# Kernel tuning notes

Hardware: AMD Instinct MI355X
Metric: run time of the kernel (lower is better)

## Reference

```python
import jax, jax.numpy as jnp
import numpy as np

N_NODES = 50000
NODE_IN, NODE_OUT, EDGE_IN = 128, 64, 32
N_EDGES = 400000
ALPHA = 0.2  # LeakyReLU negative slope
EPS = 1e-12  # F.normalize clamp


def setup_inputs() -> dict:
    key = jax.random.key(0)
    ks = jax.random.split(key, 6)
    node_fts = jax.random.normal(ks[0], (N_NODES, NODE_IN), dtype=jnp.float32)
    edge_fts = jax.random.normal(ks[1], (N_EDGES, EDGE_IN), dtype=jnp.float32)
    edges = jax.random.randint(ks[2], (2, N_EDGES), 0, N_NODES)
    # W_node: Linear(node_in, node_out); store weight as [in, out] for x @ W
    W = jax.random.normal(ks[3], (NODE_IN, NODE_OUT), dtype=jnp.float32) * (1.414 * (6.0 / (NODE_IN + NODE_OUT)) ** 0.5)
    b = jnp.zeros((NODE_OUT,), dtype=jnp.float32)
    a_node = jax.random.normal(ks[4], (2 * NODE_OUT + EDGE_IN, 1), dtype=jnp.float32) * 0.1
    scale = jnp.ones((), dtype=jnp.float32)  # MessageNorm learned scale
    return {"node_fts": node_fts, "edge_fts": edge_fts, "edges": edges,
            "W": W, "b": b, "a_node": a_node, "scale": scale}


def reference(node_fts, edge_fts, edges, W, b, a_node, scale):
    # edges: [2, E] -> reshape (row-major, as in torch) to [E, 2]
    e = edges.reshape(-1, 2)                                  # [E, 2]
    eu = jnp.concatenate([e, e[:, ::-1]], axis=0)             # undirected [2E, 2]
    ef_u = jnp.concatenate([edge_fts, edge_fts], axis=0)      # [2E, edge_in]
    src, dst = eu[:, 0], eu[:, 1]

    h_v = node_fts @ W + b                                    # [N, out]

    # per-edge attention logits: cat(h_src, h_dst, edge_ft) @ a
    feat = jnp.concatenate([h_v[src], h_v[dst], ef_u], axis=1)  # [2E, 2*out+edge_in]
    att = jnp.exp(jax.nn.leaky_relu(feat @ a_node, negative_slope=ALPHA))  # [2E, 1]

    att_sum = jax.ops.segment_sum(att, src, num_segments=N_NODES)[src]     # [2E, 1]
    att_norm = jnp.log(att / att_sum)                          # log-softmax over dst per src
    att_var = jnp.var(att_norm, ddof=1)                        # torch.var (unbiased)

    msg = jax.ops.segment_sum(h_v[dst] * att_norm, src, num_segments=N_NODES)  # [N, out]

    # MessageNorm(learn_scale=True): l2-normalize msg, rescale by ||h_v|| * scale
    msg_n = msg / jnp.maximum(jnp.linalg.norm(msg, axis=-1, keepdims=True), EPS)
    agg = msg_n * jnp.linalg.norm(h_v, axis=-1, keepdims=True) * scale

    final_embed = jnp.concatenate([h_v, agg], axis=1)          # [N, 2*out]
    return final_embed, att_var
```

## Files before the change

### kernel.cpp

```cpp
#include <hip/hip_runtime.h>

#define N_NODES 50000
#define NIN 128
#define NOUT 64
#define EIN 32
#define N_EDGES 400000
#define N_UNITS (2 * N_EDGES)
#define ALPHA 0.2f
#define CAP 64
#define N_GATHER_BLOCKS 12500

__device__ __forceinline__ int clampi(int x) {
  return min(max(x, 0), N_NODES - 1);
}

__device__ __forceinline__ unsigned bf16_lo(float f) {
  unsigned u = __float_as_uint(f);
  return (u + 0x7FFFu + ((u >> 16) & 1u)) >> 16;
}
__device__ __forceinline__ unsigned bf16_hi(float f) {
  unsigned u = __float_as_uint(f);
  return (u + 0x7FFFu + ((u >> 16) & 1u)) & 0xFFFF0000u;
}

__global__ __launch_bounds__(256) void k_gemm(
    const float* __restrict__ nf, const float* __restrict__ W,
    const float* __restrict__ b, const float* __restrict__ a,
    float* __restrict__ out, unsigned short* __restrict__ hb,
    float* __restrict__ A, float* __restrict__ B, float* __restrict__ hn) {
  __shared__ float Ws[NIN * NOUT];
  __shared__ float bs[NOUT], a1s[NOUT], a2s[NOUT];
  __shared__ float rows[4][NIN];
  int t = threadIdx.x;
#pragma unroll
  for (int n = 0; n < 32; ++n) Ws[t + n * 256] = W[t + n * 256];
  if (t < 64) { bs[t] = b[t]; a1s[t] = a[t]; a2s[t] = a[64 + t]; }
  __syncthreads();
  int j = t & 63, local = t >> 6;
  for (int v0 = blockIdx.x * 4; v0 < N_NODES; v0 += gridDim.x * 4) {
    int vload = v0 + (t >> 6);
    if (vload < N_NODES) {
      float2 p = ((const float2*)(nf + (size_t)vload * NIN))[t & 63];
      ((float2*)rows[t >> 6])[t & 63] = p;
    }
    __syncthreads();
    int v = v0 + local;
    if (v < N_NODES) {
      float acc = bs[j];
      const float* r = rows[local];
#pragma unroll
      for (int k = 0; k < NIN; k += 4) {
        float4 rk = *(const float4*)&r[k];
        acc += rk.x * Ws[(k + 0) * NOUT + j];
        acc += rk.y * Ws[(k + 1) * NOUT + j];
        acc += rk.z * Ws[(k + 2) * NOUT + j];
        acc += rk.w * Ws[(k + 3) * NOUT + j];
      }
      out[(size_t)v * 128 + j] = acc;
      hb[(size_t)v * NOUT + j] = (unsigned short)bf16_lo(acc);
      float pa = acc * a1s[j], pb = acc * a2s[j], pn = acc * acc;
      for (int o = 32; o > 0; o >>= 1) {
        pa += __shfl_down(pa, o, 64);
        pb += __shfl_down(pb, o, 64);
        pn += __shfl_down(pn, o, 64);
      }
      if (j == 0) { A[v] = pa; B[v] = pb; hn[v] = sqrtf(pn); }
    }
    __syncthreads();
  }
}

__global__ __launch_bounds__(256) void k_edge1(
    const int* __restrict__ eb, const float* __restrict__ ef,
    const float* __restrict__ a, const float* __restrict__ A,
    const float* __restrict__ B, int* __restrict__ cnt,
    unsigned* __restrict__ csr) {
  __shared__ float a3s[EIN];
  if (threadIdx.x < EIN) a3s[threadIdx.x] = a[128 + threadIdx.x];
  __syncthreads();
  int i = blockIdx.x * blockDim.x + threadIdx.x;
  if (i >= N_EDGES) return;
  int2 sd = ((const int2*)eb)[i];
  int s = clampi(sd.x), d = clampi(sd.y);
  const float4* efp = (const float4*)(ef + (size_t)i * EIN);
  float c = 0.f;
#pragma unroll
  for (int q = 0; q < 8; ++q) {
    float4 u = efp[q];
    c += u.x * a3s[4 * q + 0] + u.y * a3s[4 * q + 1] +
         u.z * a3s[4 * q + 2] + u.w * a3s[4 * q + 3];
  }
  float zf = A[s] + B[d] + c;
  float zr = A[d] + B[s] + c;
  float lf = zf > 0.f ? zf : ALPHA * zf;
  float lr = zr > 0.f ? zr : ALPHA * zr;
  int ps = atomicAdd(&cnt[s], 1);
  if (ps < CAP) csr[(size_t)s * CAP + ps] = bf16_hi(lf) | (unsigned)d;
  int pd = atomicAdd(&cnt[d], 1);
  if (pd < CAP) csr[(size_t)d * CAP + pd] = bf16_hi(lr) | (unsigned)s;
}

__global__ __launch_bounds__(256) void k_gather(
    const uint4* __restrict__ hb4, const float* __restrict__ hn,
    const int* __restrict__ cnt, const unsigned* __restrict__ csr,
    const float* __restrict__ scale_p, float* __restrict__ out,
    double* __restrict__ parts) {
  __shared__ double s1s[4], s2s[4];
  float scale = scale_p[0];
  int t = threadIdx.x;
  int w = t >> 6;
  int l = t & 63;
  int g = l >> 3;
  int p = l & 7;
  int v = blockIdx.x * 4 + w;
  int deg = min(__builtin_amdgcn_readfirstlane(cnt[v]), CAP);
  int k0 = v * CAP;
  int k1 = k0 + deg;
  float mA[8] = {0.f, 0.f, 0.f, 0.f, 0.f, 0.f, 0.f, 0.f};
  float mB[8] = {0.f, 0.f, 0.f, 0.f, 0.f, 0.f, 0.f, 0.f};
  float Se = 0.f, L1 = 0.f, L2 = 0.f;
  unsigned E = csr[k0 + g];
  for (int kb = k0; kb < k1; kb += 8) {
    unsigned C = E;
    if (kb + 8 < k1) E = csr[kb + 8 + g];
    bool valid = (kb + g) < k1;
    int idx = valid ? (int)(C & 0xFFFFu) : v;
    float lk = valid ? __uint_as_float(C & 0xFFFF0000u) : 0.f;
    float vm = valid ? 1.f : 0.f;
    uint4 q = hb4[(size_t)idx * 8 + p];
    float hv[8];
    hv[0] = __uint_as_float(q.x << 16);
    hv[1] = __uint_as_float(q.x & 0xFFFF0000u);
    hv[2] = __uint_as_float(q.y << 16);
    hv[3] = __uint_as_float(q.y & 0xFFFF0000u);
    hv[4] = __uint_as_float(q.z << 16);
    hv[5] = __uint_as_float(q.z & 0xFFFF0000u);
    hv[6] = __uint_as_float(q.w << 16);
    hv[7] = __uint_as_float(q.w & 0xFFFF0000u);
    Se += valid ? __expf(lk) : 0.f;
    L1 += lk;
    L2 += lk * lk;
#pragma unroll
    for (int c = 0; c < 8; ++c) {
      mA[c] = fmaf(hv[c], lk, mA[c]);
      mB[c] = fmaf(hv[c], vm, mB[c]);
    }
  }
  for (int o = 8; o < 64; o <<= 1) {
    Se += __shfl_xor(Se, o, 64);
    L1 += __shfl_xor(L1, o, 64);
    L2 += __shfl_xor(L2, o, 64);
  }
  float logS = (deg > 0) ? logf(Se) : 0.f;
  float mf[8];
#pragma unroll
  for (int c = 0; c < 8; ++c) mf[c] = mA[c] - logS * mB[c];
  for (int o = 8; o < 64; o <<= 1) {
#pragma unroll
    for (int c = 0; c < 8; ++c) mf[c] += __shfl_xor(mf[c], o, 64);
  }
  float nr = 0.f;
#pragma unroll
  for (int c = 0; c < 8; ++c) nr += mf[c] * mf[c];
  for (int o = 1; o < 8; o <<= 1) nr += __shfl_xor(nr, o, 64);
  nr = sqrtf(nr);
  float fac = hn[v] * scale / fmaxf(nr, 1e-12f);
  if (g == 0) {
    float4 s0 = make_float4(mf[0] * fac, mf[1] * fac, mf[2] * fac, mf[3] * fac);
    float4 s1 = make_float4(mf[4] * fac, mf[5] * fac, mf[6] * fac, mf[7] * fac);
    float* op = out + (size_t)v * 128 + 64 + p * 8;
    ((float4*)op)[0] = s0;
    ((float4*)op)[1] = s1;
  }
  if (l == 0) {
    double dls = (double)logS, dl1 = (double)L1, dl2 = (double)L2;
    double dd = (double)deg;
    s1s[w] = dl1 - dd * dls;
    s2s[w] = dl2 - 2.0 * dls * dl1 + dd * dls * dls;
  }
  __syncthreads();
  if (t == 0) {
    parts[2 * blockIdx.x] = s1s[0] + s1s[1] + s1s[2] + s1s[3];
    parts[2 * blockIdx.x + 1] = s2s[0] + s2s[1] + s2s[2] + s2s[3];
  }
}

__global__ __launch_bounds__(256) void k_var(const double* __restrict__ parts,
                                             float* __restrict__ out) {
  __shared__ double s1[256], s2[256];
  int t = threadIdx.x;
  double a1 = 0.0, a2 = 0.0;
  for (int i = t; i < N_GATHER_BLOCKS; i += 256) {
    a1 += parts[2 * i];
    a2 += parts[2 * i + 1];
  }
  s1[t] = a1;
  s2[t] = a2;
  __syncthreads();
  for (int o = 128; o > 0; o >>= 1) {
    if (t < o) {
      s1[t] += s1[t + o];
      s2[t] += s2[t + o];
    }
    __syncthreads();
  }
  if (t == 0) {
    double M = (double)N_UNITS;
    double var = (s2[0] - s1[0] * s1[0] / M) / (M - 1.0);
    out[(size_t)N_NODES * 128] = (float)var;
  }
}

extern "C" void kernel_launch(void* const* d_in, const int* in_sizes, int n_in,
                              void* d_out, int out_size, void* d_ws,
                              size_t ws_size, hipStream_t stream) {
  const float* nf = (const float*)d_in[0];
  const float* ef = (const float*)d_in[1];
  const int* eb = (const int*)d_in[2];
  const float* W = (const float*)d_in[3];
  const float* b = (const float*)d_in[4];
  const float* a = (const float*)d_in[5];
  const float* scale_p = (const float*)d_in[6];
  float* out = (float*)d_out;

  char* ws = (char*)d_ws;
  unsigned short* hb = (unsigned short*)(ws + 0);
  unsigned* csr = (unsigned*)(ws + 6400000);
  float* A = (float*)(ws + 19200000);
  float* B = (float*)(ws + 19400000);
  float* hn = (float*)(ws + 19600000);
  int* cnt = (int*)(ws + 19800000);
  double* parts = (double*)(ws + 20000000);

  hipMemsetAsync(ws + 19800000, 0, 200000, stream);

  k_gemm<<<1024, 256, 0, stream>>>(nf, W, b, a, out, hb, A, B, hn);
  k_edge1<<<(N_EDGES + 255) / 256, 256, 0, stream>>>(eb, ef, a, A, B, cnt,
                                                     csr);
  k_gather<<<N_GATHER_BLOCKS, 256, 0, stream>>>((const uint4*)hb, hn, cnt, csr,
                                                scale_p, out, parts);
  k_var<<<1, 256, 0, stream>>>(parts, out);
}
```

Before: 257.9 us.

## Hold weight column in registers and drop LDS staging in node GEMM

The node GEMM kernel now keeps each thread's 128-element weight column in registers and reads node rows straight from global memory as float4 (every lane of a wave loads the same address), so the LDS weight tile, the row staging and the per-iteration barriers are gone. Four independent accumulators shorten the FMA dependency chain, and launch bounds ask for two blocks per CU. The cost is high register pressure, about 128 VGPRs just for weights, which risks spilling or lower occupancy.

```diff
diff --git a/kernel.cpp b/kernel.cpp
--- a/kernel.cpp
+++ b/kernel.cpp
@@ -23,50 +23,54 @@
   return (u + 0x7FFFu + ((u >> 16) & 1u)) & 0xFFFF0000u;
 }
 
-__global__ __launch_bounds__(256) void k_gemm(
+__global__ __launch_bounds__(256, 2) void k_gemm(
     const float* __restrict__ nf, const float* __restrict__ W,
     const float* __restrict__ b, const float* __restrict__ a,
     float* __restrict__ out, unsigned short* __restrict__ hb,
     float* __restrict__ A, float* __restrict__ B, float* __restrict__ hn) {
-  __shared__ float Ws[NIN * NOUT];
-  __shared__ float bs[NOUT], a1s[NOUT], a2s[NOUT];
-  __shared__ float rows[4][NIN];
   int t = threadIdx.x;
-#pragma unroll
-  for (int n = 0; n < 32; ++n) Ws[t + n * 256] = W[t + n * 256];
-  if (t < 64) { bs[t] = b[t]; a1s[t] = a[t]; a2s[t] = a[64 + t]; }
-  __syncthreads();
-  int j = t & 63, local = t >> 6;
-  for (int v0 = blockIdx.x * 4; v0 < N_NODES; v0 += gridDim.x * 4) {
-    int vload = v0 + (t >> 6);
-    if (vload < N_NODES) {
-      float2 p = ((const float2*)(nf + (size_t)vload * NIN))[t & 63];
-      ((float2*)rows[t >> 6])[t & 63] = p;
-    }
-    __syncthreads();
-    int v = v0 + local;
-    if (v < N_NODES) {
-      float acc = bs[j];
-      const float* r = rows[local];
-#pragma unroll
-      for (int k = 0; k < NIN; k += 4) {
-        float4 rk = *(const float4*)&r[k];
-        acc += rk.x * Ws[(k + 0) * NOUT + j];
-        acc += rk.y * Ws[(k + 1) * NOUT + j];
-        acc += rk.z * Ws[(k + 2) * NOUT + j];
-        acc += rk.w * Ws[(k + 3) * NOUT + j];
-      }
-      out[(size_t)v * 128 + j] = acc;
-      hb[(size_t)v * NOUT + j] = (unsigned short)bf16_lo(acc);
-      float pa = acc * a1s[j], pb = acc * a2s[j], pn = acc * acc;
-      for (int o = 32; o > 0; o >>= 1) {
-        pa += __shfl_down(pa, o, 64);
-        pb += __shfl_down(pb, o, 64);
-        pn += __shfl_down(pn, o, 64);
-      }
-      if (j == 0) { A[v] = pa; B[v] = pb; hn[v] = sqrtf(pn); }
-    }
-    __syncthreads();
+  int j = t & 63, w = t >> 6;
+  float wk[NIN];
+#pragma unroll
+  for (int k = 0; k < NIN; ++k) wk[k] = W[(size_t)k * NOUT + j];
+  float bj = b[j], a1j = a[j], a2j = a[64 + j];
+  for (int v = blockIdx.x * 4 + w; v < N_NODES; v += gridDim.x * 4) {
+    const float4* rp = (const float4*)(nf + (size_t)v * NIN);
+    float ac0 = bj, ac1 = 0.f, ac2 = 0.f, ac3 = 0.f;
+#pragma unroll
+    for (int q = 0; q < 8; ++q) {
+      float4 r0 = rp[4 * q + 0];
+      float4 r1 = rp[4 * q + 1];
+      float4 r2 = rp[4 * q + 2];
+      float4 r3 = rp[4 * q + 3];
+      int k = 16 * q;
+      ac0 = fmaf(r0.x, wk[k + 0], ac0);
+      ac0 = fmaf(r0.y, wk[k + 1], ac0);
+      ac0 = fmaf(r0.z, wk[k + 2], ac0);
+      ac0 = fmaf(r0.w, wk[k + 3], ac0);
+      ac1 = fmaf(r1.x, wk[k + 4], ac1);
+      ac1 = fmaf(r1.y, wk[k + 5], ac1);
+      ac1 = fmaf(r1.z, wk[k + 6], ac1);
+      ac1 = fmaf(r1.w, wk[k + 7], ac1);
+      ac2 = fmaf(r2.x, wk[k + 8], ac2);
+      ac2 = fmaf(r2.y, wk[k + 9], ac2);
+      ac2 = fmaf(r2.z, wk[k + 10], ac2);
+      ac2 = fmaf(r2.w, wk[k + 11], ac2);
+      ac3 = fmaf(r3.x, wk[k + 12], ac3);
+      ac3 = fmaf(r3.y, wk[k + 13], ac3);
+      ac3 = fmaf(r3.z, wk[k + 14], ac3);
+      ac3 = fmaf(r3.w, wk[k + 15], ac3);
+    }
+    float acc = (ac0 + ac1) + (ac2 + ac3);
+    out[(size_t)v * 128 + j] = acc;
+    hb[(size_t)v * NOUT + j] = (unsigned short)bf16_lo(acc);
+    float pa = acc * a1j, pb = acc * a2j, pn = acc * acc;
+    for (int o = 32; o > 0; o >>= 1) {
+      pa += __shfl_down(pa, o, 64);
+      pb += __shfl_down(pb, o, 64);
+      pn += __shfl_down(pn, o, 64);
+    }
+    if (j == 0) { A[v] = pa; B[v] = pb; hn[v] = sqrtf(pn); }
   }
 }
 
```

Result: slower. 269.3 us (+4.4%).

## Keep W slices in registers and split K across waves in node GEMM

Applied to the files above, without the earlier changes.

The node GEMM no longer stages all of W in LDS. Each wave now keeps a 32-row slice of W in registers and computes partial dot products for 8 nodes at a time, and the four partials are reduced through shared memory. This cuts LDS traffic and shrinks the large LDS allocation, which should allow higher occupancy, at the cost of an extra reduction barrier and more register pressure. The node loop has no bounds guard; it relies on 50000 being divisible by 8.

```diff
diff --git a/kernel.cpp b/kernel.cpp
--- a/kernel.cpp
+++ b/kernel.cpp
@@ -28,37 +28,48 @@
     const float* __restrict__ b, const float* __restrict__ a,
     float* __restrict__ out, unsigned short* __restrict__ hb,
     float* __restrict__ A, float* __restrict__ B, float* __restrict__ hn) {
-  __shared__ float Ws[NIN * NOUT];
-  __shared__ float bs[NOUT], a1s[NOUT], a2s[NOUT];
-  __shared__ float rows[4][NIN];
+  __shared__ float rows[8][NIN];
+  __shared__ float part[4][8][NOUT];
   int t = threadIdx.x;
-#pragma unroll
-  for (int n = 0; n < 32; ++n) Ws[t + n * 256] = W[t + n * 256];
-  if (t < 64) { bs[t] = b[t]; a1s[t] = a[t]; a2s[t] = a[64 + t]; }
-  __syncthreads();
-  int j = t & 63, local = t >> 6;
-  for (int v0 = blockIdx.x * 4; v0 < N_NODES; v0 += gridDim.x * 4) {
-    int vload = v0 + (t >> 6);
-    if (vload < N_NODES) {
-      float2 p = ((const float2*)(nf + (size_t)vload * NIN))[t & 63];
-      ((float2*)rows[t >> 6])[t & 63] = p;
-    }
-    __syncthreads();
-    int v = v0 + local;
-    if (v < N_NODES) {
-      float acc = bs[j];
-      const float* r = rows[local];
-#pragma unroll
-      for (int k = 0; k < NIN; k += 4) {
-        float4 rk = *(const float4*)&r[k];
-        acc += rk.x * Ws[(k + 0) * NOUT + j];
-        acc += rk.y * Ws[(k + 1) * NOUT + j];
-        acc += rk.z * Ws[(k + 2) * NOUT + j];
-        acc += rk.w * Ws[(k + 3) * NOUT + j];
+  int w = t >> 6, j = t & 63;
+  float wq[32];
+#pragma unroll
+  for (int i = 0; i < 32; ++i) wq[i] = W[(size_t)(32 * w + i) * NOUT + j];
+  float bj = b[j], a1j = a[j], a2j = a[64 + j];
+  for (int base = blockIdx.x * 8; base < N_NODES; base += gridDim.x * 8) {
+    {
+      const float4* src =
+          (const float4*)(nf + (size_t)(base + (t >> 5)) * NIN);
+      ((float4*)rows[t >> 5])[t & 31] = src[t & 31];
+    }
+    __syncthreads();
+    float ac[8] = {0.f, 0.f, 0.f, 0.f, 0.f, 0.f, 0.f, 0.f};
+#pragma unroll
+    for (int q = 0; q < 8; ++q) {
+      float4 x[8];
+#pragma unroll
+      for (int r = 0; r < 8; ++r)
+        x[r] = ((const float4*)&rows[r][32 * w])[q];
+#pragma unroll
+      for (int r = 0; r < 8; ++r) {
+        ac[r] = fmaf(x[r].x, wq[4 * q + 0], ac[r]);
+        ac[r] = fmaf(x[r].y, wq[4 * q + 1], ac[r]);
+        ac[r] = fmaf(x[r].z, wq[4 * q + 2], ac[r]);
+        ac[r] = fmaf(x[r].w, wq[4 * q + 3], ac[r]);
       }
+    }
+#pragma unroll
+    for (int r = 0; r < 8; ++r) part[w][r][j] = ac[r];
+    __syncthreads();
+#pragma unroll
+    for (int s = 0; s < 2; ++s) {
+      int r = w + 4 * s;
+      int v = base + r;
+      float acc = bj + ((part[0][r][j] + part[1][r][j]) +
+                        (part[2][r][j] + part[3][r][j]));
       out[(size_t)v * 128 + j] = acc;
       hb[(size_t)v * NOUT + j] = (unsigned short)bf16_lo(acc);
-      float pa = acc * a1s[j], pb = acc * a2s[j], pn = acc * acc;
+      float pa = acc * a1j, pb = acc * a2j, pn = acc * acc;
       for (int o = 32; o > 0; o >>= 1) {
         pa += __shfl_down(pa, o, 64);
         pb += __shfl_down(pb, o, 64);
```

After: 234.8 us. -8.9%, faster.
